# Kernel tuning notes

Hardware: AMD Instinct MI355X
Metric: run time of the kernel (lower is better)

The kernel has to match this reference:

```python
import jax, jax.numpy as jnp
import numpy as np

B, C, H, W = 16, 64, 64, 64
MID = max(1, C // 8)


def setup_inputs() -> dict:
    key = jax.random.key(0)
    k1, k2, k3, k4, k5 = jax.random.split(key, 5)
    x = jax.random.normal(k1, (B, C, H, W), dtype=jnp.float32)
    # 1x1 conv weights (spectral-norm conv collapses to a plain [out,in] matrix
    # with a scalar-normalized weight; we use the effective weight directly)
    Wq = jax.random.normal(k2, (MID, C), dtype=jnp.float32) * 0.05
    Wk = jax.random.normal(k3, (MID, C), dtype=jnp.float32) * 0.05
    Wv = jax.random.normal(k4, (C, C), dtype=jnp.float32) * 0.05
    gamma = jax.random.normal(k5, (1,), dtype=jnp.float32) * 0.1
    return {"x": x, "Wq": Wq, "Wk": Wk, "Wv": Wv, "gamma": gamma}


def reference(x, Wq, Wk, Wv, gamma):
    b, c, h, w = x.shape
    n = h * w
    mid = Wq.shape[0]
    xf = x.reshape(b, c, n)                      # [B,C,N]
    q = jnp.einsum('mc,bcn->bnm', Wq, xf)        # [B,N,mid]
    k = jnp.einsum('mc,bcn->bmn', Wk, xf)        # [B,mid,N]
    scale = np.float32(1.0 / np.sqrt(mid))       # torch: / q.size(-1)**0.5, q last dim = mid
    attn = jax.nn.softmax(jnp.einsum('bnm,bmk->bnk', q, k) * scale, axis=-1)  # [B,N,N]
    v = jnp.einsum('oc,bcn->bon', Wv, xf)        # [B,C,N]
    # torch: bmm(v, attn^T) -> out[b,c,j] = sum_n v[b,c,n] * attn[b,j,n]
    out = jnp.einsum('bon,bjn->boj', v, attn).reshape(b, c, h, w)
    return gamma * out + x
```

## Files before the change

kernel.cpp:

```cpp
#include <hip/hip_runtime.h>
#include <hip/hip_bf16.h>

#define BATCH 16
#define CC    64
#define NN    4096
#define MIDD  8

typedef __attribute__((ext_vector_type(8)))  short short8;
typedef __attribute__((ext_vector_type(16))) float f32x16;
typedef __attribute__((ext_vector_type(2)))  int   v2i;

static __device__ __forceinline__ ushort f2bf(float f) {
    return __bfloat16_as_ushort(__float2bfloat16(f));
}

static __device__ __forceinline__ void glds16(const void* g, void* l) {
    __builtin_amdgcn_global_load_lds(
        (const __attribute__((address_space(1))) unsigned int*)g,
        (__attribute__((address_space(3))) unsigned int*)l, 16, 0, 0);
}

__global__ __launch_bounds__(256) void proj_kernel(
    const float* __restrict__ x,
    const float* __restrict__ Wq,
    const float* __restrict__ Wk,
    const float* __restrict__ Wv,
    ushort* __restrict__ qtr,
    ushort* __restrict__ ktr,
    ushort* __restrict__ v)
{
    int tid = threadIdx.x;
    int wv  = tid >> 6;
    int nl  = tid & 63;
    int g   = blockIdx.x * 64 + nl;
    int b   = g >> 12;
    int n   = g & (NN - 1);
    int wvu = __builtin_amdgcn_readfirstlane(wv);

    const float* xp = x + (size_t)b * CC * NN + n;

    float acc[20];
#pragma unroll
    for (int i = 0; i < 20; ++i) acc[i] = 0.f;

#pragma unroll 1
    for (int cc = 0; cc < 64; cc += 16) {
        float xv[16];
#pragma unroll
        for (int i = 0; i < 16; ++i) xv[i] = xp[(size_t)(cc + i) * NN];

        if (wvu == 0) {
#pragma unroll
            for (int m = 0; m < 8; ++m) {
                const float* w = Wq + m * 64 + cc;
                float a = acc[m];
#pragma unroll
                for (int i = 0; i < 16; ++i) a += w[i] * xv[i];
                acc[m] = a;
            }
#pragma unroll
            for (int m = 0; m < 8; ++m) {
                const float* w = Wk + m * 64 + cc;
                float a = acc[8 + m];
#pragma unroll
                for (int i = 0; i < 16; ++i) a += w[i] * xv[i];
                acc[8 + m] = a;
            }
#pragma unroll
            for (int m = 0; m < 4; ++m) {
                const float* w = Wv + m * 64 + cc;
                float a = acc[16 + m];
#pragma unroll
                for (int i = 0; i < 16; ++i) a += w[i] * xv[i];
                acc[16 + m] = a;
            }
        } else {
            int rb = wvu * 20 - 16;
#pragma unroll
            for (int m = 0; m < 20; ++m) {
                const float* w = Wv + (rb + m) * 64 + cc;
                float a = acc[m];
#pragma unroll
                for (int i = 0; i < 16; ++i) a += w[i] * xv[i];
                acc[m] = a;
            }
        }
    }

    const float SCLQ = 0.35355339059327373f * 1.4426950408889634f;
    if (wvu == 0) {
        union { short8 s8; ushort us[8]; } qb;
#pragma unroll
        for (int m = 0; m < 8; ++m) qb.us[m] = f2bf(acc[m] * SCLQ);
        *(short8*)(qtr + ((size_t)b * NN + n) * 8) = qb.s8;

        union { uint4 u4[2]; ushort us[16]; } kb2;
#pragma unroll
        for (int m = 0; m < 8; ++m) kb2.us[m] = f2bf(acc[8 + m]);
#pragma unroll
        for (int m = 8; m < 16; ++m) kb2.us[m] = 0;
        ushort* kd = ktr + ((size_t)b * NN + n) * 16;
        *(uint4*)kd       = kb2.u4[0];
        *(uint4*)(kd + 8) = kb2.u4[1];
#pragma unroll
        for (int i = 0; i < 4; ++i)
            v[((size_t)b * CC + i) * NN + n] = f2bf(acc[16 + i]);
    } else {
        int rb = wvu * 20 - 16;
#pragma unroll
        for (int i = 0; i < 20; ++i)
            v[((size_t)b * CC + rb + i) * NN + n] = f2bf(acc[i]);
    }
}

__global__ __launch_bounds__(256, 2) void attn_kernel(
    const ushort* __restrict__ qtr,
    const ushort* __restrict__ ktr,
    const ushort* __restrict__ v,
    const float*  __restrict__ x,
    const float*  __restrict__ gamma,
    float* __restrict__ out)
{
    __shared__ __align__(16) char lds[3 * 5120];

    int bid = blockIdx.x;
    int wg  = (bid & 7) * 64 + (bid >> 3);
    int b   = wg >> 5;
    int qt  = wg & 31;

    int tid  = threadIdx.x;
    int wv   = tid >> 6;
    int lane = tid & 63;
    int hi   = lane >> 5;
    int ql   = lane & 31;
    int q0   = qt * 128 + wv * 32;

    short8 qf = *(const short8*)(qtr + ((size_t)b * NN + q0 + ql) * 8);
    float  gm = gamma[0];
    short8 zero8 = {};
    if (hi) qf = zero8;
    asm volatile("s_waitcnt vmcnt(0)" ::: "memory");

    const ushort* kb_ = ktr + (size_t)b * NN * 16;
    const ushort* vb_ = v   + (size_t)b * CC * NN;

    int so   = tid >> 2;
    int sksl = (tid & 3) ^ (so & 3);
    const ushort* vsrc0 = vb_ + (size_t)so * NN + sksl * 8;
    const ushort* ksrc0 = kb_ + (tid >> 1) * 16 + (tid & 1) * 8;
    int vdsto = tid * 16;
    int kdsto = 4096 + tid * 16;

    int swz  = ql & 3;
    int g00  = (4 * ql + (hi ^ swz)) * 16;
    int g10  = (4 * ql + ((2 + hi) ^ swz)) * 16;
    int koff = 4096 + (2 * ql + hi) * 16;

    char* b0 = lds;
    char* b1 = lds + 5120;
    char* b2 = lds + 10240;

    f32x16 zf   = {};
    f32x16 acc0 = {};
    f32x16 acc1 = {};
    float  lsum = 0.f;

    glds16(vsrc0, b0 + vdsto);
    if (wv == 0) glds16(ksrc0, b0 + kdsto);
    glds16(vsrc0 + 32, b1 + vdsto);
    if (wv == 0) glds16(ksrc0 + 32 * 16, b1 + kdsto);

    for (int t = 0; t < 128; ++t) {
        int k2 = ((t + 2) & 127) * 32;

        __builtin_amdgcn_s_barrier();
        glds16(vsrc0 + k2, b2 + vdsto);
        if (wv == 0) {
            glds16(ksrc0 + (size_t)k2 * 16, b2 + kdsto);
            asm volatile("s_waitcnt vmcnt(4)" ::: "memory");
        } else {
            asm volatile("s_waitcnt vmcnt(2)" ::: "memory");
        }
        __builtin_amdgcn_s_barrier();
        __builtin_amdgcn_sched_barrier(0);

        short8 kfrag = *(const short8*)(b0 + koff);
        f32x16 s = __builtin_amdgcn_mfma_f32_32x32x16_bf16(kfrag, qf, zf, 0, 0, 0);

        float p[16];
#pragma unroll
        for (int r = 0; r < 16; ++r) p[r] = __builtin_amdgcn_exp2f(s[r]);
        float t0 = (p[0] + p[1]) + (p[2] + p[3]);
        float t1 = (p[4] + p[5]) + (p[6] + p[7]);
        float t2 = (p[8] + p[9]) + (p[10] + p[11]);
        float t3 = (p[12] + p[13]) + (p[14] + p[15]);
        lsum += (t0 + t1) + (t2 + t3);

        unsigned u[8];
#pragma unroll
        for (int i = 0; i < 8; ++i)
            asm("v_cvt_pk_bf16_f32 %0, %1, %2"
                : "=v"(u[i]) : "v"(p[2 * i]), "v"(p[2 * i + 1]));

        v2i r02 = __builtin_amdgcn_permlane32_swap(u[0], u[2], false, false);
        v2i r13 = __builtin_amdgcn_permlane32_swap(u[1], u[3], false, false);
        v2i r46 = __builtin_amdgcn_permlane32_swap(u[4], u[6], false, false);
        v2i r57 = __builtin_amdgcn_permlane32_swap(u[5], u[7], false, false);
        union { short8 s8; int i4[4]; } P0, P1;
        P0.i4[0] = r02.x; P0.i4[1] = r13.x; P0.i4[2] = r02.y; P0.i4[3] = r13.y;
        P1.i4[0] = r46.x; P1.i4[1] = r57.x; P1.i4[2] = r46.y; P1.i4[3] = r57.y;

        short8 va00 = *(const short8*)(b0 + g00);
        short8 va01 = *(const short8*)(b0 + 2048 + g00);
        short8 va10 = *(const short8*)(b0 + g10);
        short8 va11 = *(const short8*)(b0 + 2048 + g10);

        __builtin_amdgcn_s_setprio(1);
        acc0 = __builtin_amdgcn_mfma_f32_32x32x16_bf16(va00, P0.s8, acc0, 0, 0, 0);
        acc1 = __builtin_amdgcn_mfma_f32_32x32x16_bf16(va01, P0.s8, acc1, 0, 0, 0);
        acc0 = __builtin_amdgcn_mfma_f32_32x32x16_bf16(va10, P1.s8, acc0, 0, 0, 0);
        acc1 = __builtin_amdgcn_mfma_f32_32x32x16_bf16(va11, P1.s8, acc1, 0, 0, 0);
        __builtin_amdgcn_s_setprio(0);

        char* tp = b0; b0 = b1; b1 = b2; b2 = tp;
    }

    lsum += __shfl_xor(lsum, 32);
    float inv = gm / lsum;

#pragma unroll
    for (int r = 0; r < 16; ++r) {
        int o = (r & 3) + 8 * (r >> 2) + 4 * hi;
        size_t i0 = ((size_t)(b * CC + o)) * NN + q0 + ql;
        out[i0] = acc0[r] * inv + x[i0];
        size_t i1 = i0 + (size_t)32 * NN;
        out[i1] = acc1[r] * inv + x[i1];
    }
}

extern "C" void kernel_launch(void* const* d_in, const int* in_sizes, int n_in,
                              void* d_out, int out_size, void* d_ws, size_t ws_size,
                              hipStream_t stream) {
    const float* x     = (const float*)d_in[0];
    const float* Wq    = (const float*)d_in[1];
    const float* Wk    = (const float*)d_in[2];
    const float* Wv    = (const float*)d_in[3];
    const float* gamma = (const float*)d_in[4];
    float* out = (float*)d_out;

    ushort* qtr = (ushort*)d_ws;
    ushort* ktr = qtr + (size_t)BATCH * NN * 8;
    ushort* vws = ktr + (size_t)BATCH * NN * 16;

    proj_kernel<<<dim3((BATCH * NN) / 64), dim3(256), 0, stream>>>(x, Wq, Wk, Wv, qtr, ktr, vws);
    attn_kernel<<<dim3((BATCH * NN) / 128), dim3(256), 0, stream>>>(qtr, ktr, vws, x, gamma, out);
}
```

Baseline: 159.9 us.

## Compute softmax row sums via MFMA with ones and stage projection weights in LDS

The attention kernel drops the per-lane VALU reduction of the exponentials and instead gets row sums from two extra MFMAs that multiply a bf16 all-ones operand by the packed probabilities. The sum then reflects the bf16-rounded P, which matches what the value MFMA consumes. The V and K LDS swizzles and source addressing are also reworked. The projection kernel now stages all weights in shared memory and runs one uniform 20-row loop with float4 LDS reads, removing the branchy scalar or global weight loads. The cost is 50% more MFMA work per iteration and an LDS fill per projection block.

```diff
diff --git a/kernel.cpp b/kernel.cpp
--- a/kernel.cpp
+++ b/kernel.cpp
@@ -29,15 +29,21 @@
     ushort* __restrict__ ktr,
     ushort* __restrict__ v)
 {
+    __shared__ __align__(16) float sW[80 * 64];
+
     int tid = threadIdx.x;
-    int wv  = tid >> 6;
-    int nl  = tid & 63;
-    int g   = blockIdx.x * 64 + nl;
-    int b   = g >> 12;
-    int n   = g & (NN - 1);
-    int wvu = __builtin_amdgcn_readfirstlane(wv);
+    for (int i = tid; i < 512; i += 256) { sW[i] = Wq[i]; sW[512 + i] = Wk[i]; }
+    for (int i = tid; i < 4096; i += 256) sW[1024 + i] = Wv[i];
+    __syncthreads();
+
+    int wv = tid >> 6;
+    int nl = tid & 63;
+    int g  = blockIdx.x * 64 + nl;
+    int b  = g >> 12;
+    int n  = g & (NN - 1);
 
     const float* xp = x + (size_t)b * CC * NN + n;
+    const float* wb = sW + wv * 20 * 64;
 
     float acc[20];
 #pragma unroll
@@ -49,46 +55,21 @@
 #pragma unroll
         for (int i = 0; i < 16; ++i) xv[i] = xp[(size_t)(cc + i) * NN];
 
-        if (wvu == 0) {
-#pragma unroll
-            for (int m = 0; m < 8; ++m) {
-                const float* w = Wq + m * 64 + cc;
-                float a = acc[m];
-#pragma unroll
-                for (int i = 0; i < 16; ++i) a += w[i] * xv[i];
-                acc[m] = a;
-            }
-#pragma unroll
-            for (int m = 0; m < 8; ++m) {
-                const float* w = Wk + m * 64 + cc;
-                float a = acc[8 + m];
-#pragma unroll
-                for (int i = 0; i < 16; ++i) a += w[i] * xv[i];
-                acc[8 + m] = a;
-            }
-#pragma unroll
-            for (int m = 0; m < 4; ++m) {
-                const float* w = Wv + m * 64 + cc;
-                float a = acc[16 + m];
-#pragma unroll
-                for (int i = 0; i < 16; ++i) a += w[i] * xv[i];
-                acc[16 + m] = a;
-            }
-        } else {
-            int rb = wvu * 20 - 16;
-#pragma unroll
-            for (int m = 0; m < 20; ++m) {
-                const float* w = Wv + (rb + m) * 64 + cc;
-                float a = acc[m];
-#pragma unroll
-                for (int i = 0; i < 16; ++i) a += w[i] * xv[i];
-                acc[m] = a;
-            }
+#pragma unroll
+        for (int m = 0; m < 20; ++m) {
+            const float4* w4 = (const float4*)(wb + m * 64 + cc);
+            float4 w0 = w4[0], w1 = w4[1], w2 = w4[2], w3 = w4[3];
+            float a = acc[m];
+            a += w0.x * xv[0]  + w0.y * xv[1]  + w0.z * xv[2]  + w0.w * xv[3];
+            a += w1.x * xv[4]  + w1.y * xv[5]  + w1.z * xv[6]  + w1.w * xv[7];
+            a += w2.x * xv[8]  + w2.y * xv[9]  + w2.z * xv[10] + w2.w * xv[11];
+            a += w3.x * xv[12] + w3.y * xv[13] + w3.z * xv[14] + w3.w * xv[15];
+            acc[m] = a;
         }
     }
 
     const float SCLQ = 0.35355339059327373f * 1.4426950408889634f;
-    if (wvu == 0) {
+    if (wv == 0) {
         union { short8 s8; ushort us[8]; } qb;
 #pragma unroll
         for (int m = 0; m < 8; ++m) qb.us[m] = f2bf(acc[m] * SCLQ);
@@ -106,7 +87,7 @@
         for (int i = 0; i < 4; ++i)
             v[((size_t)b * CC + i) * NN + n] = f2bf(acc[16 + i]);
     } else {
-        int rb = wvu * 20 - 16;
+        int rb = wv * 20 - 16;
 #pragma unroll
         for (int i = 0; i < 20; ++i)
             v[((size_t)b * CC + rb + i) * NN + n] = f2bf(acc[i]);
@@ -145,25 +126,32 @@
     const ushort* vb_ = v   + (size_t)b * CC * NN;
 
     int so   = tid >> 2;
-    int sksl = (tid & 3) ^ (so & 3);
-    const ushort* vsrc0 = vb_ + (size_t)so * NN + sksl * 8;
-    const ushort* ksrc0 = kb_ + (tid >> 1) * 16 + (tid & 1) * 8;
+    int slog = (tid & 3) ^ ((so >> 1) & 3);
+    const ushort* vsrc0 = vb_ + (size_t)so * NN + slog * 8;
+    const ushort* ksrc0 = kb_ + (size_t)(tid & 31) * 16 + (tid >> 5) * 8;
     int vdsto = tid * 16;
     int kdsto = 4096 + tid * 16;
 
-    int swz  = ql & 3;
-    int g00  = (4 * ql + (hi ^ swz)) * 16;
-    int g10  = (4 * ql + ((2 + hi) ^ swz)) * 16;
-    int koff = 4096 + (2 * ql + hi) * 16;
+    int x0  = (ql >> 1) & 3;
+    int gA0 = (4 * ql + (hi ^ x0)) * 16;
+    int gA1 = (4 * ql + ((2 + hi) ^ x0)) * 16;
+    int gB0 = 2048 + gA0;
+    int gB1 = 2048 + gA1;
+    int koff = 4096 + (hi * 32 + ql) * 16;
 
     char* b0 = lds;
     char* b1 = lds + 5120;
     char* b2 = lds + 10240;
 
+    union { short8 s8; ushort us[8]; } onesu;
+#pragma unroll
+    for (int i = 0; i < 8; ++i) onesu.us[i] = 0x3F80;
+    short8 ones = onesu.s8;
+
     f32x16 zf   = {};
     f32x16 acc0 = {};
     f32x16 acc1 = {};
-    float  lsum = 0.f;
+    f32x16 accl = {};
 
     glds16(vsrc0, b0 + vdsto);
     if (wv == 0) glds16(ksrc0, b0 + kdsto);
@@ -190,11 +178,6 @@
         float p[16];
 #pragma unroll
         for (int r = 0; r < 16; ++r) p[r] = __builtin_amdgcn_exp2f(s[r]);
-        float t0 = (p[0] + p[1]) + (p[2] + p[3]);
-        float t1 = (p[4] + p[5]) + (p[6] + p[7]);
-        float t2 = (p[8] + p[9]) + (p[10] + p[11]);
-        float t3 = (p[12] + p[13]) + (p[14] + p[15]);
-        lsum += (t0 + t1) + (t2 + t3);
 
         unsigned u[8];
 #pragma unroll
@@ -210,23 +193,24 @@
         P0.i4[0] = r02.x; P0.i4[1] = r13.x; P0.i4[2] = r02.y; P0.i4[3] = r13.y;
         P1.i4[0] = r46.x; P1.i4[1] = r57.x; P1.i4[2] = r46.y; P1.i4[3] = r57.y;
 
-        short8 va00 = *(const short8*)(b0 + g00);
-        short8 va01 = *(const short8*)(b0 + 2048 + g00);
-        short8 va10 = *(const short8*)(b0 + g10);
-        short8 va11 = *(const short8*)(b0 + 2048 + g10);
+        short8 vaA0 = *(const short8*)(b0 + gA0);
+        short8 vaA1 = *(const short8*)(b0 + gA1);
+        short8 vaB0 = *(const short8*)(b0 + gB0);
+        short8 vaB1 = *(const short8*)(b0 + gB1);
 
         __builtin_amdgcn_s_setprio(1);
-        acc0 = __builtin_amdgcn_mfma_f32_32x32x16_bf16(va00, P0.s8, acc0, 0, 0, 0);
-        acc1 = __builtin_amdgcn_mfma_f32_32x32x16_bf16(va01, P0.s8, acc1, 0, 0, 0);
-        acc0 = __builtin_amdgcn_mfma_f32_32x32x16_bf16(va10, P1.s8, acc0, 0, 0, 0);
-        acc1 = __builtin_amdgcn_mfma_f32_32x32x16_bf16(va11, P1.s8, acc1, 0, 0, 0);
+        acc0 = __builtin_amdgcn_mfma_f32_32x32x16_bf16(vaA0, P0.s8, acc0, 0, 0, 0);
+        acc1 = __builtin_amdgcn_mfma_f32_32x32x16_bf16(vaB0, P0.s8, acc1, 0, 0, 0);
+        accl = __builtin_amdgcn_mfma_f32_32x32x16_bf16(ones, P0.s8, accl, 0, 0, 0);
+        acc0 = __builtin_amdgcn_mfma_f32_32x32x16_bf16(vaA1, P1.s8, acc0, 0, 0, 0);
+        acc1 = __builtin_amdgcn_mfma_f32_32x32x16_bf16(vaB1, P1.s8, acc1, 0, 0, 0);
+        accl = __builtin_amdgcn_mfma_f32_32x32x16_bf16(ones, P1.s8, accl, 0, 0, 0);
         __builtin_amdgcn_s_setprio(0);
 
         char* tp = b0; b0 = b1; b1 = b2; b2 = tp;
     }
 
-    lsum += __shfl_xor(lsum, 32);
-    float inv = gm / lsum;
+    float inv = gm / accl[0];
 
 #pragma unroll
     for (int r = 0; r < 16; ++r) {
```

After: 158.2 us. About the same (-1.0%).
